# Kernel optimization log

Hardware: AMD Instinct MI355X
Metric: run time of the kernel (lower is better)

The kernel has to match this reference:

```python
import jax, jax.numpy as jnp
import numpy as np

LN_EPS = 1e-5


def entmax15(z):
    # exact 1.5-entmax over last axis (Peters & Martins sorting algorithm)
    z = z / 2.0
    z = z - jnp.max(z, axis=-1, keepdims=True)  # shift-invariant, for stability
    zs = -jnp.sort(-z, axis=-1)                 # descending sort
    k = jnp.arange(1, z.shape[-1] + 1, dtype=z.dtype)
    mean = jnp.cumsum(zs, axis=-1) / k
    meansq = jnp.cumsum(zs * zs, axis=-1) / k
    ss = k * (meansq - jnp.square(mean))
    delta = (1.0 - ss) / k
    tau = mean - jnp.sqrt(jnp.clip(delta, 0.0))
    support = jnp.sum((tau <= zs).astype(jnp.int32), axis=-1, keepdims=True)
    tau_star = jnp.take_along_axis(tau, support - 1, axis=-1)
    return jnp.square(jnp.clip(z - tau_star, 0.0))


def layernorm_noaffine(v):
    m = jnp.mean(v, axis=-1, keepdims=True)
    var = jnp.mean(jnp.square(v - m), axis=-1, keepdims=True)
    return (v - m) / jnp.sqrt(var + LN_EPS)


def cp_mumoe(x, gate, Win, Wout):
    ones = jnp.ones(x.shape[:-1] + (1,), x.dtype)
    xb = jnp.concatenate([x, ones], axis=-1)
    z = jnp.einsum('btd,dr->btr', xb, Win) * gate  # [b,t,R]
    return jnp.einsum('btr,or->bto', z, Wout)      # [b,t,o]


def setup_inputs() -> dict:
    key = jax.random.key(0)
    ks = jax.random.split(key, 8)
    B, T, D, O, D2, E, R = 8, 2048, 1024, 4096, 1024, 16, 512
    s = lambda k, shape, scale: jax.random.normal(k, shape, jnp.float32) * scale
    return {
        'x': s(ks[0], (B, T, D), 1.0),
        'proj': s(ks[1], (D, E), D ** -0.5),
        'C1': s(ks[2], (E, R), E ** -0.5),
        'Win1': s(ks[3], (D + 1, R), D ** -0.5),
        'Wout1': s(ks[4], (O, R), R ** -0.5),
        'C2': s(ks[5], (E, R), E ** -0.5),
        'Win2': s(ks[6], (O + 1, R), O ** -0.5),
        'Wout2': s(ks[7], (D2, R), R ** -0.5),
    }


def reference(x, proj, C1, Win1, Wout1, C2, Win2, Wout2):
    # expert gating: projection -> LN (no affine) -> 1.5-entmax
    a = entmax15(layernorm_noaffine(jnp.einsum('btd,de->bte', x, proj)))  # [b,t,E]
    # layer 1: CP-decomposed expert mixture (bias folded into input mode)
    g1 = jnp.einsum('bte,er->btr', a, C1)
    h = cp_mumoe(x, g1, Win1, Wout1)
    # GELU + layer 2 reusing the same gate coefficients
    h = jax.nn.gelu(h, approximate=False)
    g2 = jnp.einsum('bte,er->btr', a, C2)
    return cp_mumoe(h, g2, Win2, Wout2)
```

## Files before the change

kernel.cpp:

```cpp
#include <hip/hip_runtime.h>
#include <hip/hip_bf16.h>
#include <math.h>
#include <stdint.h>

typedef unsigned short u16;
typedef __attribute__((ext_vector_type(8))) short bf16x8;
typedef __attribute__((ext_vector_type(4))) float f32x4;
typedef __attribute__((address_space(3))) void* as3_void;
typedef const __attribute__((address_space(1))) void* as1_cvoid;

__device__ inline u16 f2bf(float f) {
    union { float f; unsigned u; } v; v.f = f;
    unsigned r = v.u + 0x7FFFu + ((v.u >> 16) & 1u);
    return (u16)(r >> 16);
}
__device__ inline float bf2f(u16 h) {
    unsigned u = ((unsigned)h) << 16;
    return __builtin_bit_cast(float, u);
}
__device__ inline float gelu_fast(float v) {
    float t = v * fmaf(0.07135702f, v * v, 1.5957691f);
    return v / (1.f + __expf(-t));
}

template<int CTRL, int RM>
__device__ inline float dpp_mov(float v) {
    return __builtin_bit_cast(float, __builtin_amdgcn_update_dpp(
        0, __builtin_bit_cast(int, v), CTRL, RM, 0xf, false));
}
__device__ inline float wave_sum(float v) {
    v += dpp_mov<0x111, 0xf>(v);
    v += dpp_mov<0x112, 0xf>(v);
    v += dpp_mov<0x114, 0xf>(v);
    v += dpp_mov<0x118, 0xf>(v);
    v += dpp_mov<0x142, 0xa>(v);
    v += dpp_mov<0x143, 0xc>(v);
    return v;
}

__global__ __launch_bounds__(256)
void prep_all(const float* __restrict__ Win1, const float* __restrict__ Wout1,
              const float* __restrict__ Win2, const float* __restrict__ Wout2,
              u16* __restrict__ w1t, u16* __restrict__ w1o,
              u16* __restrict__ w2t, u16* __restrict__ w2o,
              float* __restrict__ b1, float* __restrict__ b2)
{
    int idx = blockIdx.x * 256 + threadIdx.x;
    if (idx < 524288) {
        int r = idx >> 10, d = idx & 1023;
        w1t[idx] = f2bf(Win1[(size_t)d * 512 + r]);
    }
    if (idx < 2097152) {
        w1o[idx] = f2bf(Wout1[idx]);
    }
    if (idx < 2097152) {
        int r = idx >> 12, o = idx & 4095;
        w2t[idx] = f2bf(Win2[(size_t)o * 512 + r]);
    }
    if (idx < 524288) {
        w2o[idx] = f2bf(Wout2[idx]);
    }
    if (idx < 512) {
        b1[idx] = Win1[(size_t)1024 * 512 + idx];
        b2[idx] = Win2[(size_t)4096 * 512 + idx];
    }
}

__global__ __launch_bounds__(256)
void k1_proj(const float* __restrict__ x, const float* __restrict__ proj,
             u16* __restrict__ xb, float* __restrict__ sbuf, int Ntok)
{
    __shared__ float plt[16 * 1024];
    const int tid = threadIdx.x;
    #pragma unroll
    for (int k = 0; k < 64; ++k) {
        int idx = k * 256 + tid;
        int e = idx & 15, d = idx >> 4;
        plt[e * 1024 + (d ^ (e << 2))] = proj[idx];
    }
    __syncthreads();

    const int lane = tid & 63;
    const int wid = tid >> 6;
    const int t0 = (blockIdx.x * 4 + wid) * 2;
    if (t0 >= Ntok) return;

    float s[16][2];
    #pragma unroll
    for (int e = 0; e < 16; ++e) { s[e][0] = 0.f; s[e][1] = 0.f; }

    #pragma unroll
    for (int j = 0; j < 4; ++j) {
        const int d0 = (j * 64 + lane) * 4;
        float4 xq[2];
        #pragma unroll
        for (int q = 0; q < 2; ++q) {
            xq[q] = *(const float4*)&x[(size_t)(t0 + q) * 1024 + d0];
            short4 h;
            h.x = (short)f2bf(xq[q].x); h.y = (short)f2bf(xq[q].y);
            h.z = (short)f2bf(xq[q].z); h.w = (short)f2bf(xq[q].w);
            *(short4*)&xb[(size_t)(t0 + q) * 1024 + d0] = h;
        }
        #pragma unroll
        for (int e = 0; e < 16; ++e) {
            float4 p = *(const float4*)&plt[e * 1024 + (d0 ^ (e << 2))];
            #pragma unroll
            for (int q = 0; q < 2; ++q) {
                s[e][q] = fmaf(xq[q].x, p.x, s[e][q]);
                s[e][q] = fmaf(xq[q].y, p.y, s[e][q]);
                s[e][q] = fmaf(xq[q].z, p.z, s[e][q]);
                s[e][q] = fmaf(xq[q].w, p.w, s[e][q]);
            }
        }
    }
    #pragma unroll
    for (int e = 0; e < 16; ++e) {
        s[e][0] = wave_sum(s[e][0]);
        s[e][1] = wave_sum(s[e][1]);
    }
    if (lane == 63) {
        #pragma unroll
        for (int q = 0; q < 2; ++q)
            #pragma unroll
            for (int c = 0; c < 4; ++c) {
                float4 o = { s[c * 4 + 0][q], s[c * 4 + 1][q],
                             s[c * 4 + 2][q], s[c * 4 + 3][q] };
                *(float4*)&sbuf[(size_t)(t0 + q) * 16 + c * 4] = o;
            }
    }
}

__global__ __launch_bounds__(256)
void k1_entmax(const float* __restrict__ sbuf, float* __restrict__ abuf, int Ntok)
{
    int t = blockIdx.x * 256 + threadIdx.x;
    if (t >= Ntok) return;
    float s[16];
    #pragma unroll
    for (int c = 0; c < 4; ++c) {
        float4 v = *(const float4*)&sbuf[(size_t)t * 16 + c * 4];
        s[c * 4 + 0] = v.x; s[c * 4 + 1] = v.y; s[c * 4 + 2] = v.z; s[c * 4 + 3] = v.w;
    }
    float mean = 0.f;
    #pragma unroll
    for (int e = 0; e < 16; ++e) mean += s[e];
    mean *= 0.0625f;
    float var = 0.f;
    #pragma unroll
    for (int e = 0; e < 16; ++e) { float d = s[e] - mean; var = fmaf(d, d, var); }
    var *= 0.0625f;
    float rstd = rsqrtf(var + 1e-5f);

    float z[16];
    #pragma unroll
    for (int e = 0; e < 16; ++e) z[e] = (s[e] - mean) * rstd * 0.5f;
    float zmax = z[0];
    #pragma unroll
    for (int e = 1; e < 16; ++e) zmax = fmaxf(zmax, z[e]);
    #pragma unroll
    for (int e = 0; e < 16; ++e) z[e] -= zmax;

    float zs[16];
    #pragma unroll
    for (int e = 0; e < 16; ++e) zs[e] = z[e];
    #pragma unroll
    for (int k = 2; k <= 16; k <<= 1) {
        #pragma unroll
        for (int j = k >> 1; j > 0; j >>= 1) {
            #pragma unroll
            for (int i = 0; i < 16; ++i) {
                int l = i ^ j;
                if (l > i) {
                    float a = zs[i], b = zs[l];
                    bool asc = ((i & k) == 0);
                    bool sw = asc ? (a > b) : (a < b);
                    if (sw) { zs[i] = b; zs[l] = a; }
                }
            }
        }
    }
    float csum = 0.f, csq = 0.f, tau_star = -3.4e38f;
    #pragma unroll
    for (int kk = 1; kk <= 16; ++kk) {
        float v = zs[16 - kk];
        csum += v; csq += v * v;
        float kf = (float)kk;
        float mn = csum / kf;
        float ms = csq / kf;
        float ss = kf * (ms - mn * mn);
        float delta = fmaxf((1.f - ss) / kf, 0.f);
        float tau = mn - sqrtf(delta);
        if (tau <= v) tau_star = tau;
    }
    #pragma unroll
    for (int c = 0; c < 4; ++c) {
        float4 o;
        float p0 = fmaxf(z[c * 4 + 0] - tau_star, 0.f);
        float p1 = fmaxf(z[c * 4 + 1] - tau_star, 0.f);
        float p2 = fmaxf(z[c * 4 + 2] - tau_star, 0.f);
        float p3 = fmaxf(z[c * 4 + 3] - tau_star, 0.f);
        o.x = p0 * p0; o.y = p1 * p1; o.z = p2 * p2; o.w = p3 * p3;
        *(float4*)&abuf[(size_t)t * 16 + c * 4] = o;
    }
}

__global__ __launch_bounds__(256)
void gcompute(const float* __restrict__ abuf, const float* __restrict__ C1,
              const float* __restrict__ C2, u16* __restrict__ g1,
              u16* __restrict__ g2, int Ntok)
{
    const int tid = threadIdx.x;
    const int lane = tid & 63;
    const int t = blockIdx.x * 4 + (tid >> 6);
    if (t >= Ntok) return;
    float a[16];
    #pragma unroll
    for (int c = 0; c < 4; ++c) {
        float4 v = *(const float4*)&abuf[(size_t)t * 16 + c * 4];
        a[c * 4 + 0] = v.x; a[c * 4 + 1] = v.y; a[c * 4 + 2] = v.z; a[c * 4 + 3] = v.w;
    }
    #pragma unroll
    for (int c8 = 0; c8 < 8; ++c8) {
        int col = c8 * 64 + lane;
        float t1 = 0.f, t2 = 0.f;
        #pragma unroll
        for (int e = 0; e < 16; ++e) {
            t1 = fmaf(a[e], C1[e * 512 + col], t1);
            t2 = fmaf(a[e], C2[e * 512 + col], t2);
        }
        g1[(size_t)t * 512 + col] = f2bf(t1);
        g2[(size_t)t * 512 + col] = f2bf(t2);
    }
}

template<int MODE>
__global__ __launch_bounds__(256, 4)
void gemm_bt(const u16* __restrict__ A, const u16* __restrict__ Bt,
             const float* __restrict__ bias, const u16* __restrict__ gmat,
             void* __restrict__ Cout, int M, int Nn, int K, int tilesN)
{
    __shared__ __align__(1024) char smem[32768];
    const int tid = threadIdx.x;
    const int lane = tid & 63;
    const int wid = tid >> 6;

    int m_t, n_t;
    {
        int bid = blockIdx.x;
        int Mtiles = gridDim.x / tilesN;
        if ((Mtiles & 7) == 0) {
            int xcd = bid & 7, loc = bid >> 3;
            int lm = loc / tilesN;
            m_t = xcd * (Mtiles >> 3) + lm;
            n_t = loc - lm * tilesN;
        } else {
            m_t = bid / tilesN;
            n_t = bid % tilesN;
        }
    }
    const int m0 = m_t * 128;
    const int n0 = n_t * 128;
    const int wm = (wid >> 1) * 64;
    const int wn = (wid & 1) * 64;

    f32x4 acc[4][4];
    #pragma unroll
    for (int i = 0; i < 4; ++i)
        #pragma unroll
        for (int j = 0; j < 4; ++j) acc[i][j] = (f32x4){0.f, 0.f, 0.f, 0.f};

    const int nsteps = K >> 6;
    for (int ks = 0; ks < nsteps; ++ks) {
        const int k0 = ks << 6;
        #pragma unroll
        for (int i = 0; i < 4; ++i) {
            int q = (wid * 4 + i) * 64 + lane;
            int row = q >> 3;
            int c = (q & 7) ^ (row & 7);
            __builtin_amdgcn_global_load_lds(
                (as1_cvoid)(A + (size_t)(m0 + row) * K + k0 + c * 8),
                (as3_void)&smem[(wid * 4 + i) * 1024], 16, 0, 0);
        }
        #pragma unroll
        for (int i = 0; i < 4; ++i) {
            int q = (wid * 4 + i) * 64 + lane;
            int row = q >> 3;
            int c = (q & 7) ^ (row & 7);
            __builtin_amdgcn_global_load_lds(
                (as1_cvoid)(Bt + (size_t)(n0 + row) * K + k0 + c * 8),
                (as3_void)&smem[16384 + (wid * 4 + i) * 1024], 16, 0, 0);
        }
        __syncthreads();
        #pragma unroll
        for (int kk = 0; kk < 2; ++kk) {
            bf16x8 af[4], bfr[4];
            const int slot = kk * 4 + (lane >> 4);
            #pragma unroll
            for (int i = 0; i < 4; ++i) {
                int row = wm + i * 16 + (lane & 15);
                af[i] = *(const bf16x8*)
                    &smem[row * 128 + ((slot ^ (row & 7)) << 4)];
            }
            #pragma unroll
            for (int j = 0; j < 4; ++j) {
                int row = wn + j * 16 + (lane & 15);
                bfr[j] = *(const bf16x8*)
                    &smem[16384 + row * 128 + ((slot ^ (row & 7)) << 4)];
            }
            #pragma unroll
            for (int i = 0; i < 4; ++i)
                #pragma unroll
                for (int j = 0; j < 4; ++j)
                    acc[i][j] = __builtin_amdgcn_mfma_f32_16x16x32_bf16(
                        af[i], bfr[j], acc[i][j], 0, 0, 0);
        }
        __syncthreads();
    }

    const int cl = lane & 15;
    const int rq = (lane >> 4) * 4;
    #pragma unroll
    for (int i = 0; i < 4; ++i) {
        #pragma unroll
        for (int j = 0; j < 4; ++j) {
            int col = n0 + wn + j * 16 + cl;
            float bv = (MODE == 1) ? bias[col] : 0.f;
            #pragma unroll
            for (int r = 0; r < 4; ++r) {
                int row = m0 + wm + i * 16 + rq + r;
                float v = acc[i][j][r];
                if (MODE == 0) {
                    ((u16*)Cout)[(size_t)row * Nn + col] = f2bf(gelu_fast(v));
                } else if (MODE == 1) {
                    v = (v + bv) * bf2f(gmat[(size_t)row * Nn + col]);
                    ((u16*)Cout)[(size_t)row * Nn + col] = f2bf(v);
                } else {
                    ((float*)Cout)[(size_t)row * Nn + col] = v;
                }
            }
        }
    }
}

extern "C" void kernel_launch(void* const* d_in, const int* in_sizes, int n_in,
                              void* d_out, int out_size, void* d_ws, size_t ws_size,
                              hipStream_t stream)
{
    const float* x     = (const float*)d_in[0];
    const float* proj  = (const float*)d_in[1];
    const float* C1    = (const float*)d_in[2];
    const float* Win1  = (const float*)d_in[3];
    const float* Wout1 = (const float*)d_in[4];
    const float* C2    = (const float*)d_in[5];
    const float* Win2  = (const float*)d_in[6];
    const float* Wout2 = (const float*)d_in[7];

    const int D = 1024, O = 4096, R = 512, D2 = 1024;
    const int Ntok = in_sizes[0] / D;

    char* ws = (char*)d_ws;
    size_t off = 0;
    auto alloc = [&](size_t bytes) -> void* {
        void* p = ws + off;
        off += (bytes + 255) & ~(size_t)255;
        return p;
    };
    u16*   z1  = (u16*)  alloc((size_t)Ntok * R * 2);
    u16*   z2  = (u16*)  alloc((size_t)Ntok * R * 2);
    u16*   w1o = (u16*)  alloc((size_t)O * R * 2);
    u16*   w2t = (u16*)  alloc((size_t)R * O * 2);
    u16*   w2o = (u16*)  alloc((size_t)D2 * R * 2);
    float* b1  = (float*)alloc(R * 4);
    float* b2  = (float*)alloc(R * 4);
    size_t persist_end = off;

    u16*   xb   = (u16*)  alloc((size_t)Ntok * D * 2);
    u16*   w1t  = (u16*)  alloc((size_t)R * D * 2);
    float* sbuf = (float*)alloc((size_t)Ntok * 16 * 4);
    float* abuf = (float*)alloc((size_t)Ntok * 16 * 4);

    size_t hAvail = (ws_size > persist_end) ? (ws_size - persist_end) : 0;
    long long chRows = (long long)(hAvail / ((size_t)O * 2));
    chRows &= ~1023LL;
    int CH = (chRows > Ntok) ? Ntok : (int)chRows;
    if (CH < 1024) CH = 1024;
    u16* hbuf = (u16*)(ws + persist_end);

    u16* g1 = z1;
    u16* g2 = z2;

    prep_all<<<(O * R + 255) / 256, 256, 0, stream>>>(
        Win1, Wout1, Win2, Wout2, w1t, w1o, w2t, w2o, b1, b2);

    k1_proj  <<<Ntok / 8, 256, 0, stream>>>(x, proj, xb, sbuf, Ntok);
    k1_entmax<<<(Ntok + 255) / 256, 256, 0, stream>>>(sbuf, abuf, Ntok);
    gcompute <<<(Ntok + 3) / 4, 256, 0, stream>>>(abuf, C1, C2, g1, g2, Ntok);

    gemm_bt<1><<<(Ntok / 128) * (R / 128), 256, 0, stream>>>(
        xb, w1t, b1, g1, z1, Ntok, R, D, R / 128);

    for (int r0 = 0; r0 < Ntok; r0 += CH) {
        int cm = Ntok - r0; if (cm > CH) cm = CH;
        gemm_bt<0><<<(cm / 128) * (O / 128), 256, 0, stream>>>(
            z1 + (size_t)r0 * R, w1o, nullptr, nullptr,
            hbuf, cm, O, R, O / 128);
        gemm_bt<1><<<(cm / 128) * (R / 128), 256, 0, stream>>>(
            hbuf, w2t, b2, g2 + (size_t)r0 * R,
            z2 + (size_t)r0 * R, cm, R, O, R / 128);
    }

    gemm_bt<2><<<(Ntok / 128) * (D2 / 128), 256, 0, stream>>>(
        z2, w2o, nullptr, nullptr, d_out, Ntok, D2, R, D2 / 128);
}
```

Baseline: 324.2 us.

## Tile weight transposes via LDS and stage GEMM bf16 epilogue through shared memory

The strided weight transposes in the prep kernel are replaced by a 32x32 LDS-tiled transpose kernel with coalesced float4 reads and short4 writes. The bf16 GEMM epilogues (GELU and bias-times-gate modes) now write results into a swizzled LDS image and then store 16-byte rows to global memory, instead of scattered 2-byte stores. In the gate mode the gate tile is prefetched into LDS with global_load_lds rather than read with scattered per-element loads. This adds an extra LDS round trip and barriers to every output tile.

```diff
diff --git a/kernel.cpp b/kernel.cpp
--- a/kernel.cpp
+++ b/kernel.cpp
@@ -39,27 +39,36 @@
 }
 
 __global__ __launch_bounds__(256)
-void prep_all(const float* __restrict__ Win1, const float* __restrict__ Wout1,
-              const float* __restrict__ Win2, const float* __restrict__ Wout2,
-              u16* __restrict__ w1t, u16* __restrict__ w1o,
-              u16* __restrict__ w2t, u16* __restrict__ w2o,
-              float* __restrict__ b1, float* __restrict__ b2)
+void prep_transpose(const float* __restrict__ src, u16* __restrict__ dst,
+                    int Rr, int Dd)
+{
+    __shared__ float t[32][33];
+    int tilesR = Rr >> 5;
+    int bi = blockIdx.x / tilesR;
+    int bj = blockIdx.x - bi * tilesR;
+    int d0 = bi * 32, r0 = bj * 32;
+    int tr = threadIdx.x >> 3, c4 = threadIdx.x & 7;
+    float4 v = *(const float4*)&src[(size_t)(d0 + tr) * Rr + r0 + c4 * 4];
+    t[tr][c4 * 4 + 0] = v.x; t[tr][c4 * 4 + 1] = v.y;
+    t[tr][c4 * 4 + 2] = v.z; t[tr][c4 * 4 + 3] = v.w;
+    __syncthreads();
+    short4 o;
+    o.x = (short)f2bf(t[c4 * 4 + 0][tr]);
+    o.y = (short)f2bf(t[c4 * 4 + 1][tr]);
+    o.z = (short)f2bf(t[c4 * 4 + 2][tr]);
+    o.w = (short)f2bf(t[c4 * 4 + 3][tr]);
+    *(short4*)&dst[(size_t)(r0 + tr) * Dd + d0 + c4 * 4] = o;
+}
+
+__global__ __launch_bounds__(256)
+void prep_cast(const float* __restrict__ Win1, const float* __restrict__ Wout1,
+               const float* __restrict__ Win2, const float* __restrict__ Wout2,
+               u16* __restrict__ w1o, u16* __restrict__ w2o,
+               float* __restrict__ b1, float* __restrict__ b2)
 {
     int idx = blockIdx.x * 256 + threadIdx.x;
-    if (idx < 524288) {
-        int r = idx >> 10, d = idx & 1023;
-        w1t[idx] = f2bf(Win1[(size_t)d * 512 + r]);
-    }
-    if (idx < 2097152) {
-        w1o[idx] = f2bf(Wout1[idx]);
-    }
-    if (idx < 2097152) {
-        int r = idx >> 12, o = idx & 4095;
-        w2t[idx] = f2bf(Win2[(size_t)o * 512 + r]);
-    }
-    if (idx < 524288) {
-        w2o[idx] = f2bf(Wout2[idx]);
-    }
+    if (idx < 2097152) w1o[idx] = f2bf(Wout1[idx]);
+    if (idx < 524288)  w2o[idx] = f2bf(Wout2[idx]);
     if (idx < 512) {
         b1[idx] = Win1[(size_t)1024 * 512 + idx];
         b2[idx] = Win2[(size_t)4096 * 512 + idx];
@@ -319,26 +328,64 @@
 
     const int cl = lane & 15;
     const int rq = (lane >> 4) * 4;
+
+    if (MODE == 2) {
+        #pragma unroll
+        for (int i = 0; i < 4; ++i)
+            #pragma unroll
+            for (int j = 0; j < 4; ++j) {
+                int col = n0 + wn + j * 16 + cl;
+                #pragma unroll
+                for (int r = 0; r < 4; ++r) {
+                    int row = m0 + wm + i * 16 + rq + r;
+                    ((float*)Cout)[(size_t)row * Nn + col] = acc[i][j][r];
+                }
+            }
+        return;
+    }
+
+    u16* img = (u16*)smem;
+    if (MODE == 1) {
+        #pragma unroll
+        for (int i8 = 0; i8 < 8; ++i8) {
+            int chunk = i8 * 256 + tid;
+            int row = chunk >> 4, gc = chunk & 15;
+            int sg = gc ^ (row & 7);
+            __builtin_amdgcn_global_load_lds(
+                (as1_cvoid)(gmat + (size_t)(m0 + row) * Nn + n0 + sg * 8),
+                (as3_void)&smem[i8 * 4096 + wid * 1024], 16, 0, 0);
+        }
+        asm volatile("s_waitcnt vmcnt(0)" ::: "memory");
+        __syncthreads();
+    }
+    float bvj[4];
+    if (MODE == 1) {
+        #pragma unroll
+        for (int j = 0; j < 4; ++j) bvj[j] = bias[n0 + wn + j * 16 + cl];
+    }
     #pragma unroll
     for (int i = 0; i < 4; ++i) {
         #pragma unroll
         for (int j = 0; j < 4; ++j) {
-            int col = n0 + wn + j * 16 + cl;
-            float bv = (MODE == 1) ? bias[col] : 0.f;
+            int lc = wn + j * 16 + cl;
             #pragma unroll
             for (int r = 0; r < 4; ++r) {
-                int row = m0 + wm + i * 16 + rq + r;
+                int lr = wm + i * 16 + rq + r;
+                int a16 = lr * 128 + (((lc >> 3) ^ (lr & 7)) << 3) + (lc & 7);
                 float v = acc[i][j][r];
-                if (MODE == 0) {
-                    ((u16*)Cout)[(size_t)row * Nn + col] = f2bf(gelu_fast(v));
-                } else if (MODE == 1) {
-                    v = (v + bv) * bf2f(gmat[(size_t)row * Nn + col]);
-                    ((u16*)Cout)[(size_t)row * Nn + col] = f2bf(v);
-                } else {
-                    ((float*)Cout)[(size_t)row * Nn + col] = v;
-                }
-            }
-        }
+                if (MODE == 0) v = gelu_fast(v);
+                else           v = (v + bvj[j]) * bf2f(img[a16]);
+                img[a16] = f2bf(v);
+            }
+        }
+    }
+    __syncthreads();
+    #pragma unroll
+    for (int g8 = 0; g8 < 8; ++g8) {
+        int chunk = g8 * 256 + tid;
+        int row = chunk >> 4, gg = chunk & 15;
+        bf16x8 vv = *(const bf16x8*)&img[row * 128 + ((gg ^ (row & 7)) << 3)];
+        *(bf16x8*)((u16*)Cout + (size_t)(m0 + row) * Nn + n0 + gg * 8) = vv;
     }
 }
 
@@ -389,8 +436,10 @@
     u16* g1 = z1;
     u16* g2 = z2;
 
-    prep_all<<<(O * R + 255) / 256, 256, 0, stream>>>(
-        Win1, Wout1, Win2, Wout2, w1t, w1o, w2t, w2o, b1, b2);
+    prep_transpose<<<(D / 32) * (R / 32), 256, 0, stream>>>(Win1, w1t, R, D);
+    prep_transpose<<<(O / 32) * (R / 32), 256, 0, stream>>>(Win2, w2t, R, O);
+    prep_cast<<<(O * R + 255) / 256, 256, 0, stream>>>(
+        Win1, Wout1, Win2, Wout2, w1o, w2o, b1, b2);
 
     k1_proj  <<<Ntok / 8, 256, 0, stream>>>(x, proj, xb, sbuf, Ntok);
     k1_entmax<<<(Ntok + 255) / 256, 256, 0, stream>>>(sbuf, abuf, Ntok);
```

Result: no change. 328.6 us (+1.4%).
